# Kernel tuning notes

Measured on AMD Instinct MI355X. Metric: run time of the kernel, lower is better.

Reference implementation:

```python
import jax, jax.numpy as jnp
import numpy as np

B, T = 64, 1024
ATTN_DIM, RNN_DIM, ENC_DIM = 128, 1024, 512
N_FILT, KSIZE = 32, 31
PAD = (KSIZE - 1) // 2


def setup_inputs() -> dict:
    key = jax.random.key(0)
    ks = jax.random.split(key, 11)
    query = jax.random.normal(ks[0], (B, RNN_DIM), dtype=jnp.float32)
    keys = jax.random.normal(ks[1], (B, T, ENC_DIM), dtype=jnp.float32)
    values = jax.random.normal(ks[2], (B, T, ENC_DIM), dtype=jnp.float32)
    attention_weights_cum = jax.random.uniform(ks[3], (B, T), dtype=jnp.float32)
    mask = jnp.zeros((B, T), dtype=bool)
    s = 0.02
    W_loc_conv = jax.random.normal(ks[4], (N_FILT, 1, KSIZE), dtype=jnp.float32) * s
    W_loc_proj = jax.random.normal(ks[5], (ATTN_DIM, N_FILT), dtype=jnp.float32) * s
    W_query = jax.random.normal(ks[6], (ATTN_DIM, RNN_DIM), dtype=jnp.float32) * s
    W_key = jax.random.normal(ks[7], (ATTN_DIM, ENC_DIM), dtype=jnp.float32) * s
    W_value = jax.random.normal(ks[8], (ENC_DIM, ENC_DIM), dtype=jnp.float32) * s
    W_attn = jax.random.normal(ks[9], (1, ATTN_DIM), dtype=jnp.float32) * s
    return {
        "query": query, "keys": keys, "values": values,
        "attention_weights_cum": attention_weights_cum, "mask": mask,
        "W_loc_conv": W_loc_conv, "W_loc_proj": W_loc_proj,
        "W_query": W_query, "W_key": W_key, "W_value": W_value, "W_attn": W_attn,
    }


def reference(query, keys, values, attention_weights_cum, mask,
              W_loc_conv, W_loc_proj, W_query, W_key, W_value, W_attn):
    # location features: conv1d over cumulative attention, (B,1,T) -> (B,N_FILT,T)
    loc = jax.lax.conv_general_dilated(
        attention_weights_cum[:, None, :], W_loc_conv,
        window_strides=(1,), padding=[(PAD, PAD)],
        dimension_numbers=("NCH", "OIH", "NCH"))
    # (B,T,N_FILT) @ W_loc_proj.T -> (B,T,ATTN_DIM)
    loc_feat = jnp.einsum("bft,af->bta", loc, W_loc_proj)
    q_proj = query @ W_query.T                      # (B, ATTN_DIM)
    k_proj = jnp.einsum("bte,ae->bta", keys, W_key)  # (B, T, ATTN_DIM)
    energies = jnp.tanh(q_proj[:, None, :] + k_proj + loc_feat)
    scores = jnp.einsum("bta,a->bt", energies, W_attn[0])  # (B, T)
    scores = jnp.where(mask, -jnp.inf, scores)
    attn = jax.nn.softmax(scores, axis=-1)
    v_proj = jnp.einsum("bte,fe->btf", values, W_value)  # (B, T, ENC_DIM)
    context = jnp.einsum("bt,btf->bf", attn, v_proj)      # (B, ENC_DIM)
    return context, attn
```

## Files before the change

kernel.cpp:

```cpp
#include <hip/hip_runtime.h>
#include <math.h>

#define B_   64
#define T_   1024
#define AD   128
#define RD   1024
#define ED   512
#define NF   32
#define KS   31
#define PADW 15

typedef short bf16x8 __attribute__((ext_vector_type(8)));
typedef float f32x4  __attribute__((ext_vector_type(4)));

typedef __attribute__((address_space(1))) unsigned gu32;
typedef __attribute__((address_space(3))) unsigned lu32;

__device__ __forceinline__ void gll16(const void* g, void* l) {
  __builtin_amdgcn_global_load_lds(
      (gu32*)(unsigned long long)g,
      (lu32*)(unsigned)(unsigned long long)l, 16, 0, 0);
}

__device__ __forceinline__ short f2bf(float x) {
  union { float f; unsigned u; } v; v.f = x;
  unsigned r = (v.u + 0x7FFFu + ((v.u >> 16) & 1u)) >> 16;
  return (short)r;
}

__device__ __forceinline__ float tanh_fast(float x) {
  float t = __expf(2.0f * x);
  return (t - 1.0f) * __builtin_amdgcn_rcpf(t + 1.0f);
}

__global__ __launch_bounds__(256) void prep_kernel(
    const float* __restrict__ Wk, const float* __restrict__ Wlp,
    const float* __restrict__ awc, const float* __restrict__ Wc,
    const float* __restrict__ query, const float* __restrict__ Wq,
    short* __restrict__ Wk16, short* __restrict__ Wlp16,
    short* __restrict__ loc_g, float* __restrict__ qp) {
  __shared__ float sh_awc[128 + KS - 1];
  __shared__ float sh_wc[NF * KS];
  __shared__ float sh_q[RD];
  __shared__ float sh_red[AD];
  const int blk = blockIdx.x, tid = threadIdx.x;

  if (blk < 68) {
    int p = blk * 256 + tid;
    const float* src; short* dst; int off;
    if (p < 16384) { src = Wk; dst = Wk16; off = p; }
    else           { src = Wlp; dst = Wlp16; off = p - 16384; }
    float4 v = *(const float4*)&src[off * 4];
    short4 h = { f2bf(v.x), f2bf(v.y), f2bf(v.z), f2bf(v.w) };
    *(short4*)&dst[off * 4] = h;
  } else if (blk < 68 + 512) {
    int cb = blk - 68;
    int b = cb >> 3, t0 = (cb & 7) * 128;
    for (int i = tid; i < NF * KS; i += 256) sh_wc[i] = Wc[i];
    if (tid < 128 + KS - 1) {
      int gt = t0 - PADW + tid;
      sh_awc[tid] = (gt >= 0 && gt < T_) ? awc[b * T_ + gt] : 0.0f;
    }
    __syncthreads();
    const int t = tid & 127, fh = (tid >> 7) * 16;
    for (int fq = 0; fq < 4; ++fq) {
      float s0 = 0.f, s1 = 0.f, s2 = 0.f, s3 = 0.f;
      const float* w0 = &sh_wc[(fh + fq * 4 + 0) * KS];
      const float* w1 = &sh_wc[(fh + fq * 4 + 1) * KS];
      const float* w2 = &sh_wc[(fh + fq * 4 + 2) * KS];
      const float* w3 = &sh_wc[(fh + fq * 4 + 3) * KS];
#pragma unroll
      for (int k = 0; k < KS; ++k) {
        float aw = sh_awc[t + k];
        s0 += w0[k] * aw; s1 += w1[k] * aw; s2 += w2[k] * aw; s3 += w3[k] * aw;
      }
      short4 h = { f2bf(s0), f2bf(s1), f2bf(s2), f2bf(s3) };
      *(short4*)&loc_g[((size_t)(b * T_ + t0 + t)) * NF + fh + fq * 4] = h;
    }
  } else {
    int b = blk - (68 + 512);
    *(float4*)&sh_q[tid * 4] = *(const float4*)&query[b * RD + tid * 4];
    __syncthreads();
    const int a = tid & 127, kh = tid >> 7;
    const float* wr = &Wq[(size_t)a * RD + kh * 512];
    const float* qr = &sh_q[kh * 512];
    float acc = 0.f;
    for (int e = 0; e < 512; e += 4) {
      float4 w = *(const float4*)&wr[e];
      acc += w.x * qr[e] + w.y * qr[e + 1] + w.z * qr[e + 2] + w.w * qr[e + 3];
    }
    if (kh == 1) sh_red[a] = acc;
    __syncthreads();
    if (kh == 0) qp[b * AD + a] = acc + sh_red[a];
  }
}

__global__ __launch_bounds__(256, 2) void scores_kernel(
    const float* __restrict__ keys, const short* __restrict__ Wk16,
    const short* __restrict__ Wlp16, const short* __restrict__ loc_g,
    const float* __restrict__ qp, const float* __restrict__ Wa,
    float* __restrict__ scores) {
  __shared__ alignas(16) short As[128 * 64];
  __shared__ alignas(16) short Bs[128 * 64];
  __shared__ float qp_s[AD], wa_s[AD];
  __shared__ float sc_s[128 * 2];

  const int tid = threadIdx.x;
  const int b = blockIdx.y, t0 = blockIdx.x * 128;
  const int lane = tid & 63, wave = tid >> 6;
  const int wm = wave >> 1, wn = wave & 1;
  const int m16 = lane & 15, s4 = lane >> 4;

  const int sr = tid >> 3;
  const int sg = tid & 7;
  const int swz = (sg ^ (sr & 7)) * 8;
  const float* kA = &keys[((size_t)(b * T_ + t0 + sr)) * ED + sg * 8];

  float4 bufA[8], bufB[8];
  auto LOADA = [&](float4 (&buf)[8], int kc) {
#pragma unroll
    for (int i = 0; i < 4; ++i) {
      const float* p = kA + (size_t)i * 32 * ED + (size_t)kc * 64;
      buf[2 * i]     = *(const float4*)p;
      buf[2 * i + 1] = *(const float4*)(p + 4);
    }
  };
  auto WRITEA = [&](float4 (&buf)[8]) {
#pragma unroll
    for (int i = 0; i < 4; ++i) {
      bf16x8 h = { f2bf(buf[2*i].x),   f2bf(buf[2*i].y),
                   f2bf(buf[2*i].z),   f2bf(buf[2*i].w),
                   f2bf(buf[2*i+1].x), f2bf(buf[2*i+1].y),
                   f2bf(buf[2*i+1].z), f2bf(buf[2*i+1].w) };
      *(bf16x8*)&As[(sr + i * 32) * 64 + swz] = h;
    }
  };

  LOADA(bufA, 0);

  if (tid < AD) { qp_s[tid] = qp[b * AD + tid]; wa_s[tid] = Wa[tid]; }

  {
    const int r = lane >> 2, cb = lane & 3;
#pragma unroll
    for (int i = 0; i < 2; ++i) {
      int row = wave * 32 + i * 16;
      gll16(&loc_g[((size_t)(b * T_ + t0 + row + r)) * NF + cb * 8],
            &As[row * 32]);
      gll16(&Wlp16[(row + r) * NF + cb * 8], &Bs[row * 32]);
    }
  }
  __syncthreads();

  f32x4 acc[4][4];
  {
    bf16x8 af[4], bfr[4];
#pragma unroll
    for (int mt = 0; mt < 4; ++mt)
      af[mt] = *(const bf16x8*)&As[(wm * 64 + mt * 16 + m16) * 32 + s4 * 8];
#pragma unroll
    for (int nt = 0; nt < 4; ++nt)
      bfr[nt] = *(const bf16x8*)&Bs[(wn * 64 + nt * 16 + m16) * 32 + s4 * 8];
#pragma unroll
    for (int mt = 0; mt < 4; ++mt)
#pragma unroll
      for (int nt = 0; nt < 4; ++nt)
        acc[mt][nt] = __builtin_amdgcn_mfma_f32_16x16x32_bf16(
            af[mt], bfr[nt], (f32x4){0.f, 0.f, 0.f, 0.f}, 0, 0, 0);
  }

  const int r8 = lane >> 3, cb8 = lane & 7;
  const int cbg = cb8 ^ r8;

  auto STAGEB = [&](int kc) {
#pragma unroll
    for (int i = 0; i < 4; ++i) {
      int row = wave * 32 + i * 8;
      gll16(&Wk16[(size_t)(row + r8) * ED + (size_t)kc * 64 + cbg * 8],
            &Bs[row * 64]);
    }
  };
  auto COMPUTE = [&]() {
#pragma unroll
    for (int kk2 = 0; kk2 < 2; ++kk2) {
      const int j = kk2 * 4 + s4;
      const int ca = (j ^ (m16 & 7)) * 8;
      bf16x8 af[4], bfr[4];
#pragma unroll
      for (int mt = 0; mt < 4; ++mt)
        af[mt] = *(const bf16x8*)&As[(wm * 64 + mt * 16 + m16) * 64 + ca];
#pragma unroll
      for (int nt = 0; nt < 4; ++nt)
        bfr[nt] = *(const bf16x8*)&Bs[(wn * 64 + nt * 16 + m16) * 64 + ca];
#pragma unroll
      for (int mt = 0; mt < 4; ++mt)
#pragma unroll
        for (int nt = 0; nt < 4; ++nt)
          acc[mt][nt] = __builtin_amdgcn_mfma_f32_16x16x32_bf16(
              af[mt], bfr[nt], acc[mt][nt], 0, 0, 0);
    }
  };

  for (int kc = 0; kc < 8; kc += 2) {
    __syncthreads();
    WRITEA(bufA);
    STAGEB(kc);
    __syncthreads();
    LOADA(bufB, kc + 1);
    COMPUTE();
    __syncthreads();
    WRITEA(bufB);
    STAGEB(kc + 1);
    __syncthreads();
    if (kc < 6) LOADA(bufA, kc + 2);
    COMPUTE();
  }

  float qv[4], wv[4];
#pragma unroll
  for (int nt = 0; nt < 4; ++nt) {
    int a = wn * 64 + nt * 16 + m16;
    qv[nt] = qp_s[a]; wv[nt] = wa_s[a];
  }
#pragma unroll
  for (int mt = 0; mt < 4; ++mt) {
#pragma unroll
    for (int r = 0; r < 4; ++r) {
      float p = 0.f;
#pragma unroll
      for (int nt = 0; nt < 4; ++nt)
        p += wv[nt] * tanh_fast(acc[mt][nt][r] + qv[nt]);
      p += __shfl_xor(p, 1); p += __shfl_xor(p, 2);
      p += __shfl_xor(p, 4); p += __shfl_xor(p, 8);
      if (m16 == 0) sc_s[(wm * 64 + mt * 16 + s4 * 4 + r) * 2 + wn] = p;
    }
  }
  __syncthreads();
  if (tid < 128)
    scores[(size_t)b * T_ + t0 + tid] = sc_s[tid * 2] + sc_s[tid * 2 + 1];
}

__global__ __launch_bounds__(256) void softmax_kernel(
    const float* __restrict__ scores, const unsigned char* __restrict__ mask,
    float* __restrict__ attn) {
  const int b = blockIdx.x, tid = threadIdx.x;
  __shared__ float redm[4], reds[4];

  float4 s4 = *(const float4*)&scores[b * T_ + tid * 4];
  uchar4 m4 = *(const uchar4*)&mask[b * T_ + tid * 4];
  if (m4.x) s4.x = -INFINITY;
  if (m4.y) s4.y = -INFINITY;
  if (m4.z) s4.z = -INFINITY;
  if (m4.w) s4.w = -INFINITY;

  float mx = fmaxf(fmaxf(s4.x, s4.y), fmaxf(s4.z, s4.w));
#pragma unroll
  for (int off = 32; off >= 1; off >>= 1) mx = fmaxf(mx, __shfl_xor(mx, off, 64));
  if ((tid & 63) == 0) redm[tid >> 6] = mx;
  __syncthreads();
  mx = fmaxf(fmaxf(redm[0], redm[1]), fmaxf(redm[2], redm[3]));

  float e0 = expf(s4.x - mx), e1 = expf(s4.y - mx);
  float e2 = expf(s4.z - mx), e3 = expf(s4.w - mx);
  float sum = e0 + e1 + e2 + e3;
#pragma unroll
  for (int off = 32; off >= 1; off >>= 1) sum += __shfl_xor(sum, off, 64);
  if ((tid & 63) == 0) reds[tid >> 6] = sum;
  __syncthreads();
  sum = reds[0] + reds[1] + reds[2] + reds[3];

  float inv = 1.0f / sum;
  float4 o4 = { e0 * inv, e1 * inv, e2 * inv, e3 * inv };
  *(float4*)&attn[b * T_ + tid * 4] = o4;
}

__global__ __launch_bounds__(256) void wvsum_kernel(
    const float* __restrict__ values, const float* __restrict__ attn,
    float* __restrict__ wvp) {
  const int tc = blockIdx.x, b = blockIdx.y, tid = threadIdx.x;
  __shared__ float at_s[32];
  if (tid < 32) at_s[tid] = attn[b * T_ + tc * 32 + tid];
  __syncthreads();
  const int e4 = tid & 127, th = tid >> 7;
  const float* vb =
      values + ((size_t)(b * T_ + tc * 32 + th * 16)) * ED + e4 * 4;
  const float* as = &at_s[th * 16];
  float4 acc = {0.f, 0.f, 0.f, 0.f};
#pragma unroll
  for (int t8 = 0; t8 < 16; t8 += 8) {
    float4 v[8];
#pragma unroll
    for (int u = 0; u < 8; ++u)
      v[u] = *(const float4*)&vb[(size_t)(t8 + u) * ED];
#pragma unroll
    for (int u = 0; u < 8; ++u) {
      float a = as[t8 + u];
      acc.x = fmaf(a, v[u].x, acc.x); acc.y = fmaf(a, v[u].y, acc.y);
      acc.z = fmaf(a, v[u].z, acc.z); acc.w = fmaf(a, v[u].w, acc.w);
    }
  }
  *(float4*)&wvp[((size_t)(b * 64 + tc * 2 + th)) * ED + e4 * 4] = acc;
}

__global__ __launch_bounds__(256) void context_kernel(
    const float* __restrict__ wvp, const float* __restrict__ Wv,
    float* __restrict__ ctx) {
  const int fq = blockIdx.x, b = blockIdx.y, tid = threadIdx.x;
  __shared__ float wv_s[ED];
  __shared__ float red[128];
  for (int e = tid; e < ED; e += 256) {
    float s = 0.f;
    const float* base = &wvp[(size_t)b * 64 * ED + e];
#pragma unroll 16
    for (int p = 0; p < 64; ++p) s += base[p * ED];
    wv_s[e] = s;
  }
  __syncthreads();
  const int fl = tid & 127, eh = tid >> 7;
  const int f = fq * 128 + fl;
  const float* wr = &Wv[(size_t)f * ED + eh * 256];
  const float* qr = &wv_s[eh * 256];
  float acc = 0.f;
  for (int e = 0; e < 256; e += 4) {
    float4 w = *(const float4*)&wr[e];
    acc += w.x * qr[e] + w.y * qr[e + 1] + w.z * qr[e + 2] + w.w * qr[e + 3];
  }
  if (eh == 1) red[fl] = acc;
  __syncthreads();
  if (eh == 0) ctx[b * ED + f] = acc + red[fl];
}

extern "C" void kernel_launch(void* const* d_in, const int* in_sizes, int n_in,
                              void* d_out, int out_size, void* d_ws, size_t ws_size,
                              hipStream_t stream) {
  const float* query = (const float*)d_in[0];
  const float* keys  = (const float*)d_in[1];
  const float* values= (const float*)d_in[2];
  const float* awc   = (const float*)d_in[3];
  const unsigned char* mask = (const unsigned char*)d_in[4];
  const float* Wc    = (const float*)d_in[5];
  const float* Wlp   = (const float*)d_in[6];
  const float* Wq    = (const float*)d_in[7];
  const float* Wk    = (const float*)d_in[8];
  const float* Wv    = (const float*)d_in[9];
  const float* Wa    = (const float*)d_in[10];

  float* ctx  = (float*)d_out;
  float* attn = (float*)d_out + B_ * ED;

  float* ws = (float*)d_ws;
  float* qp      = ws;
  float* scoresB = qp + B_ * AD;
  float* wvp     = scoresB + B_ * T_;
  short* Wk16    = (short*)(wvp + (size_t)B_ * 64 * ED);
  short* Wlp16   = Wk16 + AD * ED;
  short* loc_g   = Wlp16 + AD * NF;

  prep_kernel<<<68 + 512 + 64, 256, 0, stream>>>(Wk, Wlp, awc, Wc, query, Wq,
                                                 Wk16, Wlp16, loc_g, qp);
  scores_kernel<<<dim3(8, B_), 256, 0, stream>>>(keys, Wk16, Wlp16, loc_g,
                                                 qp, Wa, scoresB);
  softmax_kernel<<<B_, 256, 0, stream>>>(scoresB, mask, attn);
  wvsum_kernel<<<dim3(32, B_), 256, 0, stream>>>(values, attn, wvp);
  context_kernel<<<dim3(4, B_), 256, 0, stream>>>(wvp, Wv, ctx);
}
```

Baseline: 340.4 us.

## Software-pipeline scores GEMM with double-buffered B and explicit vmcnt waits

Restructures the scores kernel's K loop into an unrolled chunk pipeline. The Wk tile in LDS is double-buffered and each chunk is guarded by explicit s_waitcnt vmcnt counts and raw s_barrier instead of __syncthreads. Next-chunk global loads and LDS staging are issued before waiting on the current chunk, and MFMA blocks are wrapped in s_setprio. This aims to hide global-memory latency behind the matrix math, at the cost of more LDS and fragile hand-counted wait values that must match the number of outstanding loads.

```diff
diff --git a/kernel.cpp b/kernel.cpp
--- a/kernel.cpp
+++ b/kernel.cpp
@@ -32,6 +32,13 @@
   float t = __expf(2.0f * x);
   return (t - 1.0f) * __builtin_amdgcn_rcpf(t + 1.0f);
 }
+
+#define WAITV_(n)  asm volatile("s_waitcnt vmcnt(" #n ")" ::: "memory")
+#define WAITV(n)   WAITV_(n)
+#define WAITVL_(n) asm volatile("s_waitcnt vmcnt(" #n ") lgkmcnt(0)" ::: "memory")
+#define WAITVL(n)  WAITVL_(n)
+#define SB  __builtin_amdgcn_sched_barrier(0)
+#define BAR __builtin_amdgcn_s_barrier()
 
 __global__ __launch_bounds__(256) void prep_kernel(
     const float* __restrict__ Wk, const float* __restrict__ Wlp,
@@ -101,7 +108,7 @@
     const float* __restrict__ qp, const float* __restrict__ Wa,
     float* __restrict__ scores) {
   __shared__ alignas(16) short As[128 * 64];
-  __shared__ alignas(16) short Bs[128 * 64];
+  __shared__ alignas(16) short Bs[2][128 * 64];
   __shared__ float qp_s[AD], wa_s[AD];
   __shared__ float sc_s[128 * 2];
 
@@ -136,51 +143,18 @@
     }
   };
 
-  LOADA(bufA, 0);
-
-  if (tid < AD) { qp_s[tid] = qp[b * AD + tid]; wa_s[tid] = Wa[tid]; }
-
-  {
-    const int r = lane >> 2, cb = lane & 3;
-#pragma unroll
-    for (int i = 0; i < 2; ++i) {
-      int row = wave * 32 + i * 16;
-      gll16(&loc_g[((size_t)(b * T_ + t0 + row + r)) * NF + cb * 8],
-            &As[row * 32]);
-      gll16(&Wlp16[(row + r) * NF + cb * 8], &Bs[row * 32]);
-    }
-  }
-  __syncthreads();
-
-  f32x4 acc[4][4];
-  {
-    bf16x8 af[4], bfr[4];
-#pragma unroll
-    for (int mt = 0; mt < 4; ++mt)
-      af[mt] = *(const bf16x8*)&As[(wm * 64 + mt * 16 + m16) * 32 + s4 * 8];
-#pragma unroll
-    for (int nt = 0; nt < 4; ++nt)
-      bfr[nt] = *(const bf16x8*)&Bs[(wn * 64 + nt * 16 + m16) * 32 + s4 * 8];
-#pragma unroll
-    for (int mt = 0; mt < 4; ++mt)
-#pragma unroll
-      for (int nt = 0; nt < 4; ++nt)
-        acc[mt][nt] = __builtin_amdgcn_mfma_f32_16x16x32_bf16(
-            af[mt], bfr[nt], (f32x4){0.f, 0.f, 0.f, 0.f}, 0, 0, 0);
-  }
-
   const int r8 = lane >> 3, cb8 = lane & 7;
   const int cbg = cb8 ^ r8;
-
-  auto STAGEB = [&](int kc) {
+  auto STAGEB = [&](int kc, int half) {
 #pragma unroll
     for (int i = 0; i < 4; ++i) {
       int row = wave * 32 + i * 8;
       gll16(&Wk16[(size_t)(row + r8) * ED + (size_t)kc * 64 + cbg * 8],
-            &Bs[row * 64]);
+            &Bs[half][row * 64]);
     }
   };
-  auto COMPUTE = [&]() {
+  f32x4 acc[4][4];
+  auto COMPUTE = [&](int half) {
 #pragma unroll
     for (int kk2 = 0; kk2 < 2; ++kk2) {
       const int j = kk2 * 4 + s4;
@@ -191,30 +165,79 @@
         af[mt] = *(const bf16x8*)&As[(wm * 64 + mt * 16 + m16) * 64 + ca];
 #pragma unroll
       for (int nt = 0; nt < 4; ++nt)
-        bfr[nt] = *(const bf16x8*)&Bs[(wn * 64 + nt * 16 + m16) * 64 + ca];
+        bfr[nt] = *(const bf16x8*)&Bs[half][(wn * 64 + nt * 16 + m16) * 64 + ca];
+      __builtin_amdgcn_s_setprio(1);
 #pragma unroll
       for (int mt = 0; mt < 4; ++mt)
 #pragma unroll
         for (int nt = 0; nt < 4; ++nt)
           acc[mt][nt] = __builtin_amdgcn_mfma_f32_16x16x32_bf16(
               af[mt], bfr[nt], acc[mt][nt], 0, 0, 0);
+      __builtin_amdgcn_s_setprio(0);
     }
   };
 
-  for (int kc = 0; kc < 8; kc += 2) {
-    __syncthreads();
-    WRITEA(bufA);
-    STAGEB(kc);
-    __syncthreads();
-    LOADA(bufB, kc + 1);
-    COMPUTE();
-    __syncthreads();
-    WRITEA(bufB);
-    STAGEB(kc + 1);
-    __syncthreads();
-    if (kc < 6) LOADA(bufA, kc + 2);
-    COMPUTE();
-  }
+  if (tid < AD) qp_s[tid] = qp[b * AD + tid];
+  else          wa_s[tid - AD] = Wa[tid - AD];
+  SB;
+  {
+    const int r = lane >> 2, cbl = lane & 3;
+#pragma unroll
+    for (int i = 0; i < 2; ++i) {
+      int row = wave * 32 + i * 16;
+      gll16(&loc_g[((size_t)(b * T_ + t0 + row + r)) * NF + cbl * 8],
+            &As[row * 32]);
+      gll16(&Wlp16[(row + r) * NF + cbl * 8], &Bs[1][row * 32]);
+    }
+  }
+  SB;
+  LOADA(bufA, 0); SB;
+  STAGEB(0, 0);   SB;
+  LOADA(bufB, 1); SB;
+  WAITVL(20);
+  SB; BAR; SB;
+
+  {
+    bf16x8 af[4], bfr[4];
+#pragma unroll
+    for (int mt = 0; mt < 4; ++mt)
+      af[mt] = *(const bf16x8*)&As[(wm * 64 + mt * 16 + m16) * 32 + s4 * 8];
+#pragma unroll
+    for (int nt = 0; nt < 4; ++nt)
+      bfr[nt] = *(const bf16x8*)&Bs[1][(wn * 64 + nt * 16 + m16) * 32 + s4 * 8];
+#pragma unroll
+    for (int mt = 0; mt < 4; ++mt)
+#pragma unroll
+      for (int nt = 0; nt < 4; ++nt)
+        acc[mt][nt] = __builtin_amdgcn_mfma_f32_16x16x32_bf16(
+            af[mt], bfr[nt], (f32x4){0.f, 0.f, 0.f, 0.f}, 0, 0, 0);
+  }
+
+#define CHUNK(i, BUF, PRE, MID, DOG, DOL)                    \
+  do {                                                       \
+    BAR; SB;           \
+    WAITV(PRE); SB;                     \
+    WRITEA(BUF); SB;                                         \
+    if (DOG) STAGEB((i) + 1, ((i) + 1) & 1);                 \
+    SB;                                                      \
+    if (DOL) LOADA(BUF, (i) + 2);                            \
+    SB;                                                      \
+    WAITVL(MID);            \
+    SB; BAR; SB;                                             \
+    COMPUTE((i) & 1);                                        \
+  } while (0)
+
+  CHUNK(0, bufA, 12, 20, true,  true);
+  CHUNK(1, bufB, 12, 20, true,  true);
+  CHUNK(2, bufA, 12, 20, true,  true);
+  CHUNK(3, bufB, 12, 20, true,  true);
+  CHUNK(4, bufA, 12, 20, true,  true);
+  CHUNK(5, bufB, 12, 20, true,  true);
+  CHUNK(6, bufA, 12, 12, true,  false);
+  CHUNK(7, bufB,  4,  0, false, false);
+#undef CHUNK
+
+  __syncthreads();
 
   float qv[4], wv[4];
 #pragma unroll
```

After: 338.4 us. Within noise of the previous version (-0.6%).
